# Kernel optimization log

Measured on AMD Instinct MI355X. Metric: run time of the kernel, lower is better.

Reference implementation:

```python
import jax, jax.numpy as jnp
import numpy as np

N, E = 10000, 320000
C_IN, C_OUT = 256, 128
EPS = 1e-5


def _p(key, shape, scale=0.02):
    return (jax.random.normal(key, shape, dtype=jnp.float32) * scale)


def setup_inputs() -> dict:
    key = jax.random.key(0)
    ks = jax.random.split(key, 16)
    inp = {
        "x": jax.random.normal(ks[0], (N, C_IN), dtype=jnp.float32),
        "edge_index": jax.random.randint(ks[1], (2, E), 0, N, dtype=jnp.int64),
        # GCNConv weights (stored [in, out] so forward is x @ W)
        "W1": _p(ks[2], (C_IN, C_OUT)), "b1": jnp.zeros((C_OUT,), jnp.float32),
        "W2": _p(ks[3], (C_OUT, C_OUT)), "b2": jnp.zeros((C_OUT,), jnp.float32),
        # LayerNorms
        "ln1_g": jnp.ones((C_OUT,), jnp.float32), "ln1_b": jnp.zeros((C_OUT,), jnp.float32),
        "ln2_g": jnp.ones((C_OUT,), jnp.float32), "ln2_b": jnp.zeros((C_OUT,), jnp.float32),
        # Attention QKV
        "Wq": _p(ks[4], (C_OUT, C_OUT)), "bq": jnp.zeros((C_OUT,), jnp.float32),
        "Wk": _p(ks[5], (C_OUT, C_OUT)), "bk": jnp.zeros((C_OUT,), jnp.float32),
        "Wv": _p(ks[6], (C_OUT, C_OUT)), "bv": jnp.zeros((C_OUT,), jnp.float32),
        # shortcut Linear (in_channels != out_channels)
        "Ws": _p(ks[7], (C_IN, C_OUT)), "bs": jnp.zeros((C_OUT,), jnp.float32),
    }
    return inp


def _gcn_conv(x, W, b, src, dst, n_nodes):
    # PyG GCNConv: h = x W; add self loops; sym-normalized scatter aggregation.
    h = x @ W  # [N, out]
    loop = jnp.arange(n_nodes, dtype=src.dtype)
    s = jnp.concatenate([src, loop])
    d = jnp.concatenate([dst, loop])
    deg = jax.ops.segment_sum(jnp.ones_like(d, dtype=h.dtype), d, num_segments=n_nodes)
    dis = jnp.where(deg > 0, jax.lax.rsqrt(deg), 0.0)  # deg^-1/2
    norm = dis[s] * dis[d]  # [E+N]
    agg = jax.ops.segment_sum(h[s] * norm[:, None], d, num_segments=n_nodes)
    return agg + b


def _layer_norm(x, g, b):
    mu = jnp.mean(x, axis=-1, keepdims=True)
    var = jnp.var(x, axis=-1, keepdims=True)
    return (x - mu) * jax.lax.rsqrt(var + EPS) * g + b


def reference(x, edge_index, W1, b1, W2, b2, ln1_g, ln1_b, ln2_g, ln2_b,
              Wq, bq, Wk, bk, Wv, bv, Ws, bs):
    src, dst = edge_index[0], edge_index[1]
    n = x.shape[0]
    identity = x @ Ws + bs
    out = _gcn_conv(x, W1, b1, src, dst, n)
    out = jax.nn.silu(_layer_norm(out, ln1_g, ln1_b))  # dropout = identity (eval)
    out = _gcn_conv(out, W2, b2, src, dst, n)
    out = _layer_norm(out, ln2_g, ln2_b)
    # dense self-attention over all nodes
    q = out @ Wq + bq
    k = out @ Wk + bk
    v = out @ Wv + bv
    scale = np.sqrt(out.shape[-1]).astype(np.float32)
    attn = jax.nn.softmax(q @ k.T / scale, axis=-1)  # [N, N]
    out = attn @ v + out
    return jax.nn.silu(out + identity)
```

## Files before the change

kernel.cpp:

```cpp
#include <hip/hip_runtime.h>
#include <hip/hip_bf16.h>

typedef unsigned short u16;
typedef unsigned int u32;
typedef __bf16 bf16x8 __attribute__((ext_vector_type(8)));
typedef float f32x4 __attribute__((ext_vector_type(4)));

#define MFMA16(a, b, c) __builtin_amdgcn_mfma_f32_16x16x32_bf16(a, b, c, 0, 0, 0)

static __device__ __forceinline__ u16 f2b(float f) {
  u32 u = __float_as_uint(f);
  return (u16)((u + 0x7FFFu + ((u >> 16) & 1u)) >> 16);
}
static __device__ __forceinline__ float blo(u32 u) { return __uint_as_float(u << 16); }
static __device__ __forceinline__ float bhi(u32 u) { return __uint_as_float(u & 0xffff0000u); }
static __device__ __forceinline__ u32 packtrunc(float a, float b) {
  return (__float_as_uint(a) >> 16) | (__float_as_uint(b) & 0xffff0000u);
}
static __device__ __forceinline__ bf16x8 mk8(u32 a, u32 b, u32 c, u32 d) {
  union { u32 u[4]; bf16x8 v; } t; t.u[0] = a; t.u[1] = b; t.u[2] = c; t.u[3] = d; return t.v;
}

static __device__ __forceinline__ void async_copy16(void* lds, const void* gp) {
  __builtin_amdgcn_global_load_lds(
      (const __attribute__((address_space(1))) unsigned int*)gp,
      (__attribute__((address_space(3))) unsigned int*)lds, 16, 0, 0);
}

__global__ void prep_kernel(const int* __restrict__ dst, int* __restrict__ degi, int E,
                            const float* __restrict__ x, u16* __restrict__ xb, int n4,
                            const float* __restrict__ W1, const float* __restrict__ Ws,
                            const float* __restrict__ W2, const float* __restrict__ Wq,
                            const float* __restrict__ Wk, const float* __restrict__ Wv,
                            u16* __restrict__ wout) {
  int t = blockIdx.x * 256 + threadIdx.x;
  if (t < E) { atomicAdd(&degi[dst[t]], 1); return; }
  int t2 = t - E;
  if (t2 < n4) {
    float4 v = *(const float4*)&x[t2 * 4];
    ushort4 o;
    o.x = f2b(v.x); o.y = f2b(v.y); o.z = f2b(v.z); o.w = f2b(v.w);
    *(ushort4*)&xb[t2 * 4] = o;
    return;
  }
  int u = t2 - n4;
  if (u >= 131072) return;
  const float* src; int K, base, loc;
  if (u < 65536) {
    if (u < 32768) { src = W1; base = 0; } else { src = Ws; base = 32768; }
    loc = u - base; K = 256;
  } else {
    int seg = (u - 65536) >> 14;
    src = (seg == 0) ? W2 : (seg == 1) ? Wq : (seg == 2) ? Wk : Wv;
    base = 65536 + seg * 16384; loc = u & 16383; K = 128;
  }
  int k = loc >> 7, c = loc & 127;
  wout[base + c * K + k] = f2b(src[loc]);
}

__global__ void dis_start_kernel(const int* __restrict__ degi, float* __restrict__ d,
                                 int* __restrict__ startb, int* __restrict__ counter, int N) {
  int i = blockIdx.x * 256 + threadIdx.x;
  int lane = threadIdx.x & 63;
  int dg = (i < N) ? degi[i] : 0;
  if (i < N) d[i] = rsqrtf((float)dg + 1.0f);
  int x = dg;
#pragma unroll
  for (int ofs = 1; ofs < 64; ofs <<= 1) {
    int y = __shfl_up(x, ofs, 64);
    if (lane >= ofs) x += y;
  }
  int waveTotal = __shfl(x, 63, 64);
  int base = 0;
  if (lane == 63) base = atomicAdd(counter, waveTotal);
  base = __shfl(base, 63, 64);
  if (i < N) startb[i] = base + x - dg;
}

__global__ __launch_bounds__(256) void mid_kernel(
    const int* __restrict__ src, const int* __restrict__ dstp, const int* __restrict__ startb,
    int* __restrict__ cursor, int* __restrict__ adj, int E, int Gg,
    const u16* __restrict__ A, const u16* __restrict__ Wa, const u16* __restrict__ Wb,
    const float* __restrict__ bsb, u16* __restrict__ outa, float* __restrict__ outb, int M)
{
  if ((int)blockIdx.x >= Gg) {
    int e = (blockIdx.x - Gg) * 256 + threadIdx.x;
    if (e < E) {
      int d = dstp[e];
      int p = atomicAdd(&cursor[d], 1);
      adj[startb[d] + p] = src[e];
    }
    return;
  }
  int wv = threadIdx.x >> 6;
  int lane = threadIdx.x & 63;
  int col = lane & 15, quad = lane >> 4;
  int row0 = (blockIdx.x * 2 + (wv >> 1)) * 16;
  if (row0 >= M) return;
  int cb = (wv & 1) * 64;
  int ar = row0 + col; if (ar > M - 1) ar = M - 1;
  const u16* ap = A + (size_t)ar * 256 + quad * 8;
  f32x4 Oa[4], Ob[4];
#pragma unroll
  for (int i = 0; i < 4; i++) {
    Oa[i][0] = 0.f; Oa[i][1] = 0.f; Oa[i][2] = 0.f; Oa[i][3] = 0.f;
    Ob[i] = Oa[i];
  }
#pragma unroll
  for (int k0 = 0; k0 < 256; k0 += 32) {
    bf16x8 aA = *(const bf16x8*)(ap + k0);
#pragma unroll
    for (int nb = 0; nb < 4; nb++) {
      size_t wofs = (size_t)(cb + nb * 16 + col) * 256 + k0 + quad * 8;
      Oa[nb] = MFMA16(aA, *(const bf16x8*)(Wa + wofs), Oa[nb]);
      Ob[nb] = MFMA16(aA, *(const bf16x8*)(Wb + wofs), Ob[nb]);
    }
  }
#pragma unroll
  for (int nb = 0; nb < 4; nb++) {
    int ch = cb + nb * 16 + col;
    float bv = bsb[ch];
#pragma unroll
    for (int r = 0; r < 4; r++) {
      int row = row0 + quad * 4 + r;
      if (row >= M) continue;
      outa[(size_t)row * 128 + ch] = f2b(Oa[nb][r]);
      outb[(size_t)row * 128 + ch] = Ob[nb][r] + bv;
    }
  }
}

static __device__ __forceinline__ void gather_one_row(
    const u16* __restrict__ h, const float* __restrict__ dis,
    const int* __restrict__ adj, const int* __restrict__ startb, const int* __restrict__ degi,
    const float* __restrict__ bias, const float* __restrict__ g, const float* __restrict__ beta,
    u16* AoRow, float* curOut, int row, int N, int do_silu)
{
  int lane = threadIdx.x & 63;
  int c2 = lane * 2;
  float o0 = 0.f, o1 = 0.f;
  if (row < N) {
    int st = startb[row], dg = degi[row];
    float v0 = 0.f, v1 = 0.f;
    for (int base = 0; base < dg; base += 64) {
      int nb = min(64, dg - base);
      int myadj = 0; float mydis = 0.f;
      if (lane < nb) { myadj = adj[st + base + lane]; mydis = dis[myadj]; }
      int jj = 0;
      for (; jj + 8 <= nb; jj += 8) {
        int s0 = __shfl(myadj, jj),     s1 = __shfl(myadj, jj + 1);
        int s2 = __shfl(myadj, jj + 2), s3 = __shfl(myadj, jj + 3);
        int s4 = __shfl(myadj, jj + 4), s5 = __shfl(myadj, jj + 5);
        int s6 = __shfl(myadj, jj + 6), s7 = __shfl(myadj, jj + 7);
        float w0 = __shfl(mydis, jj),     w1 = __shfl(mydis, jj + 1);
        float w2 = __shfl(mydis, jj + 2), w3 = __shfl(mydis, jj + 3);
        float w4 = __shfl(mydis, jj + 4), w5 = __shfl(mydis, jj + 5);
        float w6 = __shfl(mydis, jj + 6), w7 = __shfl(mydis, jj + 7);
        u32 a0 = *(const u32*)&h[(size_t)s0 * 128 + c2];
        u32 a1 = *(const u32*)&h[(size_t)s1 * 128 + c2];
        u32 a2 = *(const u32*)&h[(size_t)s2 * 128 + c2];
        u32 a3 = *(const u32*)&h[(size_t)s3 * 128 + c2];
        u32 a4 = *(const u32*)&h[(size_t)s4 * 128 + c2];
        u32 a5 = *(const u32*)&h[(size_t)s5 * 128 + c2];
        u32 a6 = *(const u32*)&h[(size_t)s6 * 128 + c2];
        u32 a7 = *(const u32*)&h[(size_t)s7 * 128 + c2];
        v0 += w0 * blo(a0); v1 += w0 * bhi(a0);
        v0 += w1 * blo(a1); v1 += w1 * bhi(a1);
        v0 += w2 * blo(a2); v1 += w2 * bhi(a2);
        v0 += w3 * blo(a3); v1 += w3 * bhi(a3);
        v0 += w4 * blo(a4); v1 += w4 * bhi(a4);
        v0 += w5 * blo(a5); v1 += w5 * bhi(a5);
        v0 += w6 * blo(a6); v1 += w6 * bhi(a6);
        v0 += w7 * blo(a7); v1 += w7 * bhi(a7);
      }
      for (; jj < nb; jj++) {
        int s = __shfl(myadj, jj);
        float wv = __shfl(mydis, jj);
        u32 a = *(const u32*)&h[(size_t)s * 128 + c2];
        v0 += wv * blo(a); v1 += wv * bhi(a);
      }
    }
    float dd = dis[row];
    u32 aself = *(const u32*)&h[(size_t)row * 128 + c2];
    v0 = (v0 + dd * blo(aself)) * dd + bias[c2];
    v1 = (v1 + dd * bhi(aself)) * dd + bias[c2 + 1];
    float s = v0 + v1;
#pragma unroll
    for (int d = 32; d > 0; d >>= 1) s += __shfl_xor(s, d, 64);
    float mu = s * (1.0f / 128.0f);
    float d0 = v0 - mu, d1 = v1 - mu;
    float q = d0 * d0 + d1 * d1;
#pragma unroll
    for (int d = 32; d > 0; d >>= 1) q += __shfl_xor(q, d, 64);
    float rstd = rsqrtf(q * (1.0f / 128.0f) + 1e-5f);
    o0 = d0 * rstd * g[c2]     + beta[c2];
    o1 = d1 * rstd * g[c2 + 1] + beta[c2 + 1];
    if (do_silu) {
      o0 = o0 / (1.f + __expf(-o0));
      o1 = o1 / (1.f + __expf(-o1));
    }
    if (curOut) *(float2*)&curOut[(size_t)row * 128 + c2] = make_float2(o0, o1);
  }
  *(u32*)&AoRow[c2] = (u32)f2b(o0) | ((u32)f2b(o1) << 16);
}

__global__ __launch_bounds__(1024) void gather_gemm1(
    const u16* __restrict__ h, const float* __restrict__ dis,
    const int* __restrict__ adj, const int* __restrict__ startb, const int* __restrict__ degi,
    const float* __restrict__ b1, const float* __restrict__ g1, const float* __restrict__ be1,
    const u16* __restrict__ W2t, u16* __restrict__ h2, int N)
{
  __shared__ __align__(16) u16 Ao[16 * 136];
  int wv = threadIdx.x >> 6;
  int row0 = blockIdx.x * 16;
  gather_one_row(h, dis, adj, startb, degi, b1, g1, be1, &Ao[wv * 136], nullptr,
                 row0 + wv, N, 1);
  __syncthreads();
  if (wv >= 8) return;
  int lane = threadIdx.x & 63;
  int col = lane & 15, quad = lane >> 4;
  f32x4 acc; acc[0] = 0.f; acc[1] = 0.f; acc[2] = 0.f; acc[3] = 0.f;
#pragma unroll
  for (int ks = 0; ks < 4; ks++) {
    bf16x8 aA = *(const bf16x8*)&Ao[col * 136 + ks * 32 + quad * 8];
    const u16* bp = W2t + (size_t)(wv * 16 + col) * 128 + ks * 32 + quad * 8;
    acc = MFMA16(aA, *(const bf16x8*)bp, acc);
  }
  int ch = wv * 16 + col;
#pragma unroll
  for (int r = 0; r < 4; r++) {
    int row = row0 + quad * 4 + r;
    if (row < N) h2[(size_t)row * 128 + ch] = f2b(acc[r]);
  }
}

__global__ __launch_bounds__(1024) void gather_gemm_qkv(
    const u16* __restrict__ h2, const float* __restrict__ dis,
    const int* __restrict__ adj, const int* __restrict__ startb, const int* __restrict__ degi,
    const float* __restrict__ b2, const float* __restrict__ g2, const float* __restrict__ be2,
    const u16* __restrict__ Wqt, const u16* __restrict__ Wkt, const u16* __restrict__ Wvt,
    const float* __restrict__ bq, const float* __restrict__ bk, const float* __restrict__ bvb,
    float* __restrict__ cur, u16* __restrict__ q_out, u16* __restrict__ k_out,
    u16* __restrict__ v_out, int N, int NP, float qscale)
{
  __shared__ __align__(16) u16 Ao[16 * 136];
  int wv = threadIdx.x >> 6;
  int row0 = blockIdx.x * 16;
  gather_one_row(h2, dis, adj, startb, degi, b2, g2, be2, &Ao[wv * 136], cur,
                 row0 + wv, N, 0);
  __syncthreads();
  int lane = threadIdx.x & 63;
  int col = lane & 15, quad = lane >> 4;
  {
    const u16* Wt = (wv < 8) ? Wqt : Wkt;
    const float* bb = (wv < 8) ? bq : bk;
    int cb = (wv & 7) * 16;
    f32x4 acc; acc[0] = 0.f; acc[1] = 0.f; acc[2] = 0.f; acc[3] = 0.f;
#pragma unroll
    for (int ks = 0; ks < 4; ks++) {
      bf16x8 aA = *(const bf16x8*)&Ao[col * 136 + ks * 32 + quad * 8];
      const u16* bp = Wt + (size_t)(cb + col) * 128 + ks * 32 + quad * 8;
      acc = MFMA16(aA, *(const bf16x8*)bp, acc);
    }
    int ch = cb + col;
    float bv = bb[ch];
    if (wv < 8) {
#pragma unroll
      for (int r = 0; r < 4; r++) {
        int row = row0 + quad * 4 + r;
        if (row < N) q_out[(size_t)row * 128 + ch] = f2b((acc[r] + bv) * qscale);
      }
    } else {
#pragma unroll
      for (int r = 0; r < 4; r++) {
        int row = row0 + quad * 4 + r;
        if (row < N) k_out[(size_t)row * 128 + ch] = f2b(acc[r] + bv);
      }
    }
  }
  if (wv < 8) {
    int cb = wv * 16;
    f32x4 acc; acc[0] = 0.f; acc[1] = 0.f; acc[2] = 0.f; acc[3] = 0.f;
#pragma unroll
    for (int ks = 0; ks < 4; ks++) {
      bf16x8 aA = *(const bf16x8*)&Ao[col * 136 + ks * 32 + quad * 8];
      const u16* bp = Wvt + (size_t)(cb + col) * 128 + ks * 32 + quad * 8;
      acc = MFMA16(aA, *(const bf16x8*)bp, acc);
    }
    int ch = cb + col;
    float bv = bvb[ch];
#pragma unroll
    for (int r = 0; r < 4; r++) {
      int row = row0 + quad * 4 + r;
      if (row < N) {
        int rb = row & 31;
        int slot = (((rb >> 2) & 3) << 3) + ((rb >> 4) << 2) + (rb & 3);
        v_out[(size_t)ch * NP + (row & ~31) + slot] = f2b(acc[r] + bv);
      }
    }
  }
}

__global__ __launch_bounds__(256, 3) void flash_part(
    const u16* __restrict__ qb, const u16* __restrict__ kb, const u16* __restrict__ vt,
    u16* __restrict__ Opart, float* __restrict__ lpart,
    int N, int NP, int NPB, int CHUNK)
{
  __shared__ __align__(16) u16 Kl[3][32 * 128];
  __shared__ __align__(16) u16 Vl[3][128 * 32];
  int tid = threadIdx.x;
  int w = tid >> 6, lane = tid & 63;
  int col = lane & 15, quad = lane >> 4;
  int h8 = col & 7;
  int ks = blockIdx.y;
  int kstart = ks * CHUNK;
  int qbase = blockIdx.x * 128 + w * 32;

  bf16x8 aQ[2][4];
#pragma unroll
  for (int rg = 0; rg < 2; rg++) {
    int qr = qbase + rg * 16 + col; if (qr > N - 1) qr = N - 1;
    const u16* qp = qb + (size_t)qr * 128 + quad * 8;
    aQ[rg][0] = *(const bf16x8*)(qp);
    aQ[rg][1] = *(const bf16x8*)(qp + 32);
    aQ[rg][2] = *(const bf16x8*)(qp + 64);
    aQ[rg][3] = *(const bf16x8*)(qp + 96);
  }

  f32x4 O[2][8];
#pragma unroll
  for (int rg = 0; rg < 2; rg++)
#pragma unroll
    for (int i = 0; i < 8; i++) { O[rg][i][0] = 0.f; O[rg][i][1] = 0.f; O[rg][i][2] = 0.f; O[rg][i][3] = 0.f; }
  float lr0 = 0.f, lr1 = 0.f;

  int l16 = lane >> 4, c16 = lane & 15;
  int vch = lane >> 2, vc4 = lane & 3;

  auto stage = [&](int buf, int k0) {
#pragma unroll
    for (int i = 0; i < 2; i++) {
      int rl = w * 8 + i * 4 + l16;
      int cg = c16 ^ (rl & 7);
      async_copy16(&Kl[buf][(w * 8 + i * 4) * 128], kb + (size_t)(k0 + rl) * 128 + cg * 8);
    }
#pragma unroll
    for (int i = 0; i < 2; i++) {
      int ch = w * 32 + i * 16 + vch;
      int cg = vc4 ^ ((ch >> 1) & 3);
      async_copy16(&Vl[buf][(w * 32 + i * 16) * 32], vt + (size_t)ch * NP + k0 + cg * 8);
    }
  };

  int KT = (min(CHUNK, NP - kstart)) >> 5;
  stage(0, kstart);
  if (KT > 1) stage(1, kstart + 32);

  int buf = 0, sbuf = 2;
  for (int kt = 0; kt < KT; kt++) {
    int k0 = kstart + (kt << 5);
    if (kt + 1 < KT) asm volatile("s_waitcnt vmcnt(4)\n\ts_barrier" ::: "memory");
    else             asm volatile("s_waitcnt vmcnt(0)\n\ts_barrier" ::: "memory");
    if (kt + 2 < KT) stage(sbuf, k0 + 64);

    const u16* Kb = &Kl[buf][0];
    const u16* Vb = &Vl[buf][0];

    f32x4 sT[2][2];
#pragma unroll
    for (int kg = 0; kg < 2; kg++) {
      const u16* kr = Kb + (kg * 16 + col) * 128;
      bf16x8 kf0 = *(const bf16x8*)(kr + (((0 + quad) ^ h8) << 3));
      bf16x8 kf1 = *(const bf16x8*)(kr + (((4 + quad) ^ h8) << 3));
      bf16x8 kf2 = *(const bf16x8*)(kr + (((8 + quad) ^ h8) << 3));
      bf16x8 kf3 = *(const bf16x8*)(kr + (((12 + quad) ^ h8) << 3));
      f32x4 s0; s0[0] = 0.f; s0[1] = 0.f; s0[2] = 0.f; s0[3] = 0.f;
      f32x4 s1 = s0;
      s0 = MFMA16(kf0, aQ[0][0], s0); s1 = MFMA16(kf0, aQ[1][0], s1);
      s0 = MFMA16(kf1, aQ[0][1], s0); s1 = MFMA16(kf1, aQ[1][1], s1);
      s0 = MFMA16(kf2, aQ[0][2], s0); s1 = MFMA16(kf2, aQ[1][2], s1);
      s0 = MFMA16(kf3, aQ[0][3], s0); s1 = MFMA16(kf3, aQ[1][3], s1);
      sT[kg][0] = s0; sT[kg][1] = s1;
    }
    if (k0 + 32 > N) {
#pragma unroll
      for (int kg = 0; kg < 2; kg++) {
        int kbase = k0 + kg * 16 + quad * 4;
#pragma unroll
        for (int r = 0; r < 4; r++) {
          if (kbase + r >= N) { sT[kg][0][r] = -1e30f; sT[kg][1][r] = -1e30f; }
        }
      }
    }
    u32 plo[2][2], phi[2][2];
#pragma unroll
    for (int kg = 0; kg < 2; kg++) {
      float p00 = __expf(sT[kg][0][0]), p01 = __expf(sT[kg][0][1]);
      float p02 = __expf(sT[kg][0][2]), p03 = __expf(sT[kg][0][3]);
      float p10 = __expf(sT[kg][1][0]), p11 = __expf(sT[kg][1][1]);
      float p12 = __expf(sT[kg][1][2]), p13 = __expf(sT[kg][1][3]);
      lr0 += p00 + p01 + p02 + p03;
      lr1 += p10 + p11 + p12 + p13;
      plo[kg][0] = packtrunc(p00, p01); phi[kg][0] = packtrunc(p02, p03);
      plo[kg][1] = packtrunc(p10, p11); phi[kg][1] = packtrunc(p12, p13);
    }
    bf16x8 bP[2];
    bP[0] = mk8(plo[0][0], phi[0][0], plo[1][0], phi[1][0]);
    bP[1] = mk8(plo[0][1], phi[0][1], plo[1][1], phi[1][1]);
#pragma unroll
    for (int nb = 0; nb < 8; nb++) {
      int ch = nb * 16 + col;
      const u16* vr = Vb + ch * 32;
      bf16x8 vf = *(const bf16x8*)(vr + ((quad ^ ((ch >> 1) & 3)) << 3));
      O[0][nb] = MFMA16(vf, bP[0], O[0][nb]);
      O[1][nb] = MFMA16(vf, bP[1], O[1][nb]);
    }
    buf = (buf == 2) ? 0 : buf + 1;
    sbuf = (sbuf == 2) ? 0 : sbuf + 1;
  }

  lr0 += __shfl_xor(lr0, 16, 64); lr0 += __shfl_xor(lr0, 32, 64);
  lr1 += __shfl_xor(lr1, 16, 64); lr1 += __shfl_xor(lr1, 32, 64);
  if (lane < 16) {
    lpart[(size_t)ks * NPB + qbase + lane] = lr0;
    lpart[(size_t)ks * NPB + qbase + 16 + lane] = lr1;
  }
#pragma unroll
  for (int rg = 0; rg < 2; rg++) {
    int row = qbase + rg * 16 + col;
    u16* dstrow = Opart + ((size_t)ks * NPB + row) * 128 + quad * 4;
#pragma unroll
    for (int nb = 0; nb < 8; nb++) {
      u32 w01 = (u32)f2b(O[rg][nb][0]) | ((u32)f2b(O[rg][nb][1]) << 16);
      u32 w23 = (u32)f2b(O[rg][nb][2]) | ((u32)f2b(O[rg][nb][3]) << 16);
      *(uint2*)(dstrow + nb * 16) = make_uint2(w01, w23);
    }
  }
}

__global__ __launch_bounds__(256) void attn_combine(
    const u16* __restrict__ Opart, const float* __restrict__ lpart,
    const float* __restrict__ out2, const float* __restrict__ ident, float* __restrict__ out,
    int N, int NPB, int S)
{
  int row = blockIdx.x * 4 + (threadIdx.x >> 6);
  int c2 = (threadIdx.x & 63) * 2;
  if (row >= N) return;
  float num0 = 0.f, num1 = 0.f, den = 0.f;
  for (int u = 0; u < S; u++) {
    u32 b = *(const u32*)&Opart[((size_t)u * NPB + row) * 128 + c2];
    num0 += blo(b); num1 += bhi(b);
    den += lpart[(size_t)u * NPB + row];
  }
  size_t idx = (size_t)row * 128 + c2;
  float rinv = 1.0f / den;
  float2 o2 = *(const float2*)&out2[idx];
  float2 id = *(const float2*)&ident[idx];
  float v0 = num0 * rinv + o2.x + id.x;
  float v1 = num1 * rinv + o2.y + id.y;
  v0 = v0 / (1.f + __expf(-v0));
  v1 = v1 / (1.f + __expf(-v1));
  *(float2*)&out[idx] = make_float2(v0, v1);
}

extern "C" void kernel_launch(void* const* d_in, const int* in_sizes, int n_in,
                              void* d_out, int out_size, void* d_ws, size_t ws_size,
                              hipStream_t stream) {
  const float* x   = (const float*)d_in[0];
  const int*   ei  = (const int*)d_in[1];
  const float* W1  = (const float*)d_in[2];
  const float* b1  = (const float*)d_in[3];
  const float* W2  = (const float*)d_in[4];
  const float* b2  = (const float*)d_in[5];
  const float* g1  = (const float*)d_in[6];
  const float* be1 = (const float*)d_in[7];
  const float* g2  = (const float*)d_in[8];
  const float* be2 = (const float*)d_in[9];
  const float* Wq  = (const float*)d_in[10];
  const float* bq  = (const float*)d_in[11];
  const float* Wk  = (const float*)d_in[12];
  const float* bk  = (const float*)d_in[13];
  const float* Wv  = (const float*)d_in[14];
  const float* bv  = (const float*)d_in[15];
  const float* Wsw = (const float*)d_in[16];
  const float* bs  = (const float*)d_in[17];

  const int CIN = 256, C = 128;
  int N = in_sizes[0] / CIN;
  int E = in_sizes[1] / 2;
  int NP = (N + 63) & ~63;
  int NPB = (N + 127) & ~127;
  const int* src = ei;
  const int* dstp = ei + E;

  const int S = 8;
  int tiles = NP / 64;
  int CHUNK = ((tiles + S - 1) / S) * 64;

  char* w = (char*)d_ws;
  size_t off = 0;
  auto alloc = [&](size_t bytes) -> void* {
    void* p = w + off;
    off = (off + bytes + 255) & ~(size_t)255;
    return p;
  };
  int*   degi   = (int*)alloc((size_t)N * 4);
  int*   cursor = (int*)alloc((size_t)N * 4);
  int*   counter= (int*)alloc(256);
  size_t zlen   = off;
  float* disb   = (float*)alloc((size_t)N * 4);
  int*   startb = (int*)alloc((size_t)N * 4);
  int*   adj    = (int*)alloc((size_t)E * 4);
  u16*   h      = (u16*)alloc((size_t)N * C * 2);
  u16*   h2     = (u16*)alloc((size_t)N * C * 2);
  float* ident  = (float*)alloc((size_t)N * C * 4);
  float* cur    = (float*)alloc((size_t)N * C * 4);
  u16*   xb     = (u16*)alloc((size_t)N * CIN * 2);
  u16*   wt     = (u16*)alloc((size_t)131072 * 2);
  u16*   qbb    = (u16*)alloc((size_t)N * C * 2);
  u16*   kbb    = (u16*)alloc((size_t)NP * C * 2);
  u16*   vt     = (u16*)alloc((size_t)C * NP * 2);
  u16*   Opart  = (u16*)alloc((size_t)S * NPB * C * 2);
  float* lpart  = (float*)alloc((size_t)S * NPB * 4);

  u16* wt1 = wt;
  u16* wts = wt + 32768;
  u16* wt2 = wt + 65536;
  u16* wtq = wt + 81920;
  u16* wtk = wt + 98304;
  u16* wtv = wt + 114688;

  hipMemsetAsync(degi, 0, zlen, stream);

  int n4 = N * CIN / 4;
  int ptot = E + n4 + 131072;
  prep_kernel<<<(ptot + 255) / 256, 256, 0, stream>>>(dstp, degi, E, x, xb, n4,
                                                      W1, Wsw, W2, Wq, Wk, Wv, wt);
  int gN = (N + 255) / 256;
  dis_start_kernel<<<gN, 256, 0, stream>>>(degi, disb, startb, counter, N);

  int rowtiles = (N + 15) / 16;
  int Gg = (rowtiles + 1) / 2;
  int gE = (E + 255) / 256;
  mid_kernel<<<Gg + gE, 256, 0, stream>>>(src, dstp, startb, cursor, adj, E, Gg,
                                          xb, wt1, wts, bs, h, ident, N);

  int gRows = (N + 15) / 16;
  gather_gemm1<<<gRows, 1024, 0, stream>>>(h, disb, adj, startb, degi, b1, g1, be1,
                                           wt2, h2, N);

  const float qscale = 0.08838834764831845f;
  gather_gemm_qkv<<<gRows, 1024, 0, stream>>>(h2, disb, adj, startb, degi, b2, g2, be2,
                                              wtq, wtk, wtv, bq, bk, bv,
                                              cur, qbb, kbb, vt, N, NP, qscale);

  dim3 fg(NPB / 128, S);
  flash_part<<<fg, 256, 0, stream>>>(qbb, kbb, vt, Opart, lpart, N, NP, NPB, CHUNK);
  attn_combine<<<(N + 3) / 4, 256, 0, stream>>>(Opart, lpart, cur, ident,
                                                (float*)d_out, N, NPB, S);
}
```

Baseline: 269.0 us.

## Switch flash attention inner loop from 16x16x32 to 32x32x16 MFMA

Rewrites the flash_part kernel to use 32x32x16 bf16 MFMA instructions for both the QK^T score tile and the PV accumulation, instead of pairs of 16x16x32 MFMAs. The V output permutation written by the projection kernel is changed to match the new MFMA operand layout. The goal is fewer MFMA issues and LDS fragment loads per tile, plus a simpler row-sum reduction. The cost is larger per-lane accumulator registers, which could affect occupancy.

```diff
diff --git a/kernel.cpp b/kernel.cpp
--- a/kernel.cpp
+++ b/kernel.cpp
@@ -5,8 +5,10 @@
 typedef unsigned int u32;
 typedef __bf16 bf16x8 __attribute__((ext_vector_type(8)));
 typedef float f32x4 __attribute__((ext_vector_type(4)));
+typedef float f32x16 __attribute__((ext_vector_type(16)));
 
 #define MFMA16(a, b, c) __builtin_amdgcn_mfma_f32_16x16x32_bf16(a, b, c, 0, 0, 0)
+#define MFMA32(a, b, c) __builtin_amdgcn_mfma_f32_32x32x16_bf16(a, b, c, 0, 0, 0)
 
 static __device__ __forceinline__ u16 f2b(float f) {
   u32 u = __float_as_uint(f);
@@ -294,7 +296,8 @@
       int row = row0 + quad * 4 + r;
       if (row < N) {
         int rb = row & 31;
-        int slot = (((rb >> 2) & 3) << 3) + ((rb >> 4) << 2) + (rb & 3);
+        int slot = (((rb >> 4) & 1) << 4) + (((rb >> 2) & 1) << 3)
+                 + (((rb >> 3) & 1) << 2) + (rb & 3);
         v_out[(size_t)ch * NP + (row & ~31) + slot] = f2b(acc[r] + bv);
       }
     }
@@ -310,29 +313,23 @@
   __shared__ __align__(16) u16 Vl[3][128 * 32];
   int tid = threadIdx.x;
   int w = tid >> 6, lane = tid & 63;
-  int col = lane & 15, quad = lane >> 4;
-  int h8 = col & 7;
+  int q32 = lane & 31, hh = lane >> 5;
   int ks = blockIdx.y;
   int kstart = ks * CHUNK;
   int qbase = blockIdx.x * 128 + w * 32;
 
-  bf16x8 aQ[2][4];
-#pragma unroll
-  for (int rg = 0; rg < 2; rg++) {
-    int qr = qbase + rg * 16 + col; if (qr > N - 1) qr = N - 1;
-    const u16* qp = qb + (size_t)qr * 128 + quad * 8;
-    aQ[rg][0] = *(const bf16x8*)(qp);
-    aQ[rg][1] = *(const bf16x8*)(qp + 32);
-    aQ[rg][2] = *(const bf16x8*)(qp + 64);
-    aQ[rg][3] = *(const bf16x8*)(qp + 96);
-  }
-
-  f32x4 O[2][8];
-#pragma unroll
-  for (int rg = 0; rg < 2; rg++)
-#pragma unroll
-    for (int i = 0; i < 8; i++) { O[rg][i][0] = 0.f; O[rg][i][1] = 0.f; O[rg][i][2] = 0.f; O[rg][i][3] = 0.f; }
-  float lr0 = 0.f, lr1 = 0.f;
+  int qr = qbase + q32; if (qr > N - 1) qr = N - 1;
+  const u16* qp = qb + (size_t)qr * 128 + hh * 8;
+  bf16x8 aQ[8];
+#pragma unroll
+  for (int i = 0; i < 8; i++) aQ[i] = *(const bf16x8*)(qp + 16 * i);
+
+  f32x16 O[4];
+#pragma unroll
+  for (int c = 0; c < 4; c++)
+#pragma unroll
+    for (int i = 0; i < 16; i++) O[c][i] = 0.f;
+  float lr = 0.f;
 
   int l16 = lane >> 4, c16 = lane & 15;
   int vch = lane >> 2, vc4 = lane & 3;
@@ -366,74 +363,60 @@
     const u16* Kb = &Kl[buf][0];
     const u16* Vb = &Vl[buf][0];
 
-    f32x4 sT[2][2];
-#pragma unroll
-    for (int kg = 0; kg < 2; kg++) {
-      const u16* kr = Kb + (kg * 16 + col) * 128;
-      bf16x8 kf0 = *(const bf16x8*)(kr + (((0 + quad) ^ h8) << 3));
-      bf16x8 kf1 = *(const bf16x8*)(kr + (((4 + quad) ^ h8) << 3));
-      bf16x8 kf2 = *(const bf16x8*)(kr + (((8 + quad) ^ h8) << 3));
-      bf16x8 kf3 = *(const bf16x8*)(kr + (((12 + quad) ^ h8) << 3));
-      f32x4 s0; s0[0] = 0.f; s0[1] = 0.f; s0[2] = 0.f; s0[3] = 0.f;
-      f32x4 s1 = s0;
-      s0 = MFMA16(kf0, aQ[0][0], s0); s1 = MFMA16(kf0, aQ[1][0], s1);
-      s0 = MFMA16(kf1, aQ[0][1], s0); s1 = MFMA16(kf1, aQ[1][1], s1);
-      s0 = MFMA16(kf2, aQ[0][2], s0); s1 = MFMA16(kf2, aQ[1][2], s1);
-      s0 = MFMA16(kf3, aQ[0][3], s0); s1 = MFMA16(kf3, aQ[1][3], s1);
-      sT[kg][0] = s0; sT[kg][1] = s1;
+    f32x16 sT;
+#pragma unroll
+    for (int i = 0; i < 16; i++) sT[i] = 0.f;
+    const u16* kr = Kb + q32 * 128;
+#pragma unroll
+    for (int i = 0; i < 8; i++) {
+      bf16x8 kf = *(const bf16x8*)(kr + (((2 * i + hh) ^ (q32 & 7)) << 3));
+      sT = MFMA32(kf, aQ[i], sT);
     }
     if (k0 + 32 > N) {
 #pragma unroll
-      for (int kg = 0; kg < 2; kg++) {
-        int kbase = k0 + kg * 16 + quad * 4;
+      for (int t = 0; t < 4; t++)
 #pragma unroll
         for (int r = 0; r < 4; r++) {
-          if (kbase + r >= N) { sT[kg][0][r] = -1e30f; sT[kg][1][r] = -1e30f; }
+          if (k0 + r + 8 * t + 4 * hh >= N) sT[4 * t + r] = -1e30f;
         }
-      }
-    }
-    u32 plo[2][2], phi[2][2];
-#pragma unroll
-    for (int kg = 0; kg < 2; kg++) {
-      float p00 = __expf(sT[kg][0][0]), p01 = __expf(sT[kg][0][1]);
-      float p02 = __expf(sT[kg][0][2]), p03 = __expf(sT[kg][0][3]);
-      float p10 = __expf(sT[kg][1][0]), p11 = __expf(sT[kg][1][1]);
-      float p12 = __expf(sT[kg][1][2]), p13 = __expf(sT[kg][1][3]);
-      lr0 += p00 + p01 + p02 + p03;
-      lr1 += p10 + p11 + p12 + p13;
-      plo[kg][0] = packtrunc(p00, p01); phi[kg][0] = packtrunc(p02, p03);
-      plo[kg][1] = packtrunc(p10, p11); phi[kg][1] = packtrunc(p12, p13);
-    }
-    bf16x8 bP[2];
-    bP[0] = mk8(plo[0][0], phi[0][0], plo[1][0], phi[1][0]);
-    bP[1] = mk8(plo[0][1], phi[0][1], plo[1][1], phi[1][1]);
-#pragma unroll
-    for (int nb = 0; nb < 8; nb++) {
-      int ch = nb * 16 + col;
+    }
+    u32 p[8];
+#pragma unroll
+    for (int k = 0; k < 8; k++) {
+      float e0 = __expf(sT[2 * k]);
+      float e1 = __expf(sT[2 * k + 1]);
+      lr += e0 + e1;
+      p[k] = packtrunc(e0, e1);
+    }
+    bf16x8 bP0 = mk8(p[0], p[1], p[2], p[3]);
+    bf16x8 bP1 = mk8(p[4], p[5], p[6], p[7]);
+#pragma unroll
+    for (int c = 0; c < 4; c++) {
+      int ch = c * 32 + q32;
       const u16* vr = Vb + ch * 32;
-      bf16x8 vf = *(const bf16x8*)(vr + ((quad ^ ((ch >> 1) & 3)) << 3));
-      O[0][nb] = MFMA16(vf, bP[0], O[0][nb]);
-      O[1][nb] = MFMA16(vf, bP[1], O[1][nb]);
+      int sw = (ch >> 1) & 3;
+      bf16x8 vf0 = *(const bf16x8*)(vr + (((0 + hh) ^ sw) << 3));
+      bf16x8 vf1 = *(const bf16x8*)(vr + (((2 + hh) ^ sw) << 3));
+      O[c] = MFMA32(vf0, bP0, O[c]);
+      O[c] = MFMA32(vf1, bP1, O[c]);
     }
     buf = (buf == 2) ? 0 : buf + 1;
     sbuf = (sbuf == 2) ? 0 : sbuf + 1;
   }
 
-  lr0 += __shfl_xor(lr0, 16, 64); lr0 += __shfl_xor(lr0, 32, 64);
-  lr1 += __shfl_xor(lr1, 16, 64); lr1 += __shfl_xor(lr1, 32, 64);
-  if (lane < 16) {
-    lpart[(size_t)ks * NPB + qbase + lane] = lr0;
-    lpart[(size_t)ks * NPB + qbase + 16 + lane] = lr1;
-  }
-#pragma unroll
-  for (int rg = 0; rg < 2; rg++) {
-    int row = qbase + rg * 16 + col;
-    u16* dstrow = Opart + ((size_t)ks * NPB + row) * 128 + quad * 4;
-#pragma unroll
-    for (int nb = 0; nb < 8; nb++) {
-      u32 w01 = (u32)f2b(O[rg][nb][0]) | ((u32)f2b(O[rg][nb][1]) << 16);
-      u32 w23 = (u32)f2b(O[rg][nb][2]) | ((u32)f2b(O[rg][nb][3]) << 16);
-      *(uint2*)(dstrow + nb * 16) = make_uint2(w01, w23);
+  lr += __shfl_xor(lr, 32, 64);
+  if (lane < 32) lpart[(size_t)ks * NPB + qbase + lane] = lr;
+
+  int row = qbase + q32;
+  u16* dstrow = Opart + ((size_t)ks * NPB + row) * 128;
+#pragma unroll
+  for (int c = 0; c < 4; c++) {
+#pragma unroll
+    for (int t = 0; t < 4; t++) {
+      int ch = c * 32 + 8 * t + 4 * hh;
+      u32 w01 = (u32)f2b(O[c][4 * t + 0]) | ((u32)f2b(O[c][4 * t + 1]) << 16);
+      u32 w23 = (u32)f2b(O[c][4 * t + 2]) | ((u32)f2b(O[c][4 * t + 3]) << 16);
+      *(uint2*)(dstrow + ch) = make_uint2(w01, w23);
     }
   }
 }
```

Result: no change. 274.0 us (+1.9%).
